# Performance work log

Hardware: AMD Instinct MI355X
Metric: run time of the kernel (lower is better)

## Reference

```python
import jax, jax.numpy as jnp
import numpy as np


def setup_inputs() -> dict:
    key = jax.random.key(0)
    k1, k2 = jax.random.split(key)
    features = jax.random.normal(k1, (2048, 2, 4096), dtype=jnp.float32)
    labels = jax.random.randint(k2, (2048,), 0, 8)  # int labels 0..7
    return {"features": features, "labels": labels}


def reference(features, labels):
    # contrast_mode='one': anchors are view 0 only
    anchor = features[:, 0]                     # [N, d]
    N, d = anchor.shape
    logp = jax.nn.log_softmax(anchor, axis=1)    # [N, d]
    p = jnp.exp(logp)                            # softmax probs

    # Pairwise symmetric KL via one matmul.
    # F.kl_div(log p, q, reduction='batchmean') on 1-D vectors of length d
    # = sum_k q_k (log q_k - log p_k) / d, so
    # sym_kl(i,j) = (C[i,i] + C[j,j] - C[i,j] - C[j,i]) / (2d)
    # where C[i,j] = sum_k p_i[k] * logp_j[k].
    C = p @ logp.T                               # [N, N]
    diag = jnp.diagonal(C)                       # sum p log p per row
    M = (diag[:, None] + diag[None, :] - C - C.T) / (2.0 * d)

    triu = jnp.triu(jnp.ones((N, N), dtype=bool), k=1)  # unordered pairs i<j
    same = labels[:, None] == labels[None, :]
    same_sum = jnp.sum(jnp.where(triu & same, M, 0.0))
    diff_sum = jnp.sum(jnp.where(triu & ~same, M, 0.0))
    return same_sum / diff_sum
```

## Files before the change

### kernel.cpp

```cpp
#include <hip/hip_runtime.h>
#include <cmath>

#define N_ROWS 2048
#define DIM 4096
#define ROW_STRIDE 8192
#define NCLS 8

__device__ __forceinline__ float wred_sum(float v){
  #pragma unroll
  for(int o=32;o>0;o>>=1) v += __shfl_xor(v,o,64);
  return v;
}
__device__ __forceinline__ float wred_max(float v){
  #pragma unroll
  for(int o=32;o>0;o>>=1) v = fmaxf(v,__shfl_xor(v,o,64));
  return v;
}

__global__ __launch_bounds__(256) void k1_rowstats(
    const float* __restrict__ feat, float* __restrict__ lse,
    float* __restrict__ diag, float* __restrict__ zero_region){
  const int t = threadIdx.x;
  const int row = blockIdx.x;
  if(row < 64){
    float4* z = (float4*)zero_region;
    z[row*256 + t] = make_float4(0.f,0.f,0.f,0.f);
  }
  const float4* x4 = (const float4*)(feat + (size_t)row * ROW_STRIDE);
  float4 v[4];
  #pragma unroll
  for(int k=0;k<4;k++) v[k] = x4[t + k*256];

  __shared__ float red[4];
  float m = -INFINITY;
  #pragma unroll
  for(int k=0;k<4;k++)
    m = fmaxf(m, fmaxf(fmaxf(v[k].x,v[k].y), fmaxf(v[k].z,v[k].w)));
  m = wred_max(m);
  if((t & 63)==0) red[t>>6] = m;
  __syncthreads();
  m = fmaxf(fmaxf(red[0],red[1]), fmaxf(red[2],red[3]));
  __syncthreads();
  float s = 0.f;
  #pragma unroll
  for(int k=0;k<4;k++)
    s += __expf(v[k].x - m) + __expf(v[k].y - m)
       + __expf(v[k].z - m) + __expf(v[k].w - m);
  s = wred_sum(s);
  if((t&63)==0) red[t>>6] = s;
  __syncthreads();
  s = red[0]+red[1]+red[2]+red[3];
  __syncthreads();
  const float l = m + __logf(s);
  float dg = 0.f;
  #pragma unroll
  for(int k=0;k<4;k++){
    float a=v[k].x-l, b=v[k].y-l, c=v[k].z-l, d2=v[k].w-l;
    dg += a*__expf(a) + b*__expf(b) + c*__expf(c) + d2*__expf(d2);
  }
  dg = wred_sum(dg);
  if((t&63)==0) red[t>>6] = dg;
  __syncthreads();
  if(t==0){
    lse[row] = l;
    diag[row] = red[0]+red[1]+red[2]+red[3];
  }
}

__global__ __launch_bounds__(256) void k2_accum(
    const float* __restrict__ feat, const float* __restrict__ lse,
    const int* __restrict__ labels,
    float* __restrict__ Pbuf, float* __restrict__ Lbuf){
  const int d = blockIdx.x * 256 + threadIdx.x;
  const int r0 = blockIdx.y * 64;
  float P0=0,P1=0,P2=0,P3=0,P4=0,P5=0,P6=0,P7=0;
  float L0=0,L1=0,L2=0,L3=0,L4=0,L5=0,L6=0,L7=0;
  const float* col = feat + (size_t)r0 * ROW_STRIDE + d;
  #pragma unroll 4
  for(int i=0;i<64;i++){
    const int r = r0 + i;
    float x = col[(size_t)i * ROW_STRIDE];
    float v = x - lse[r];
    float e = __expf(v);
    int lab = __builtin_amdgcn_readfirstlane(labels[r]);
    switch(lab){
      case 0: P0+=e; L0+=v; break;
      case 1: P1+=e; L1+=v; break;
      case 2: P2+=e; L2+=v; break;
      case 3: P3+=e; L3+=v; break;
      case 4: P4+=e; L4+=v; break;
      case 5: P5+=e; L5+=v; break;
      case 6: P6+=e; L6+=v; break;
      default: P7+=e; L7+=v; break;
    }
  }
  atomicAdd(&Pbuf[0*DIM+d],P0); atomicAdd(&Lbuf[0*DIM+d],L0);
  atomicAdd(&Pbuf[1*DIM+d],P1); atomicAdd(&Lbuf[1*DIM+d],L1);
  atomicAdd(&Pbuf[2*DIM+d],P2); atomicAdd(&Lbuf[2*DIM+d],L2);
  atomicAdd(&Pbuf[3*DIM+d],P3); atomicAdd(&Lbuf[3*DIM+d],L3);
  atomicAdd(&Pbuf[4*DIM+d],P4); atomicAdd(&Lbuf[4*DIM+d],L4);
  atomicAdd(&Pbuf[5*DIM+d],P5); atomicAdd(&Lbuf[5*DIM+d],L5);
  atomicAdd(&Pbuf[6*DIM+d],P6); atomicAdd(&Lbuf[6*DIM+d],L6);
  atomicAdd(&Pbuf[7*DIM+d],P7); atomicAdd(&Lbuf[7*DIM+d],L7);
}

__global__ __launch_bounds__(256) void k3_final(
    const float* __restrict__ diag, const int* __restrict__ labels,
    const float* __restrict__ Pbuf, const float* __restrict__ Lbuf,
    float* __restrict__ out){
  const int t = threadIdx.x;
  const int wave = t>>6, lane = t&63;
  double Dl[8]; int Nl[8];
  #pragma unroll
  for(int c=0;c<8;c++){ Dl[c]=0.0; Nl[c]=0; }
  for(int i=t;i<N_ROWS;i+=256){
    int lab = labels[i];
    double dg = (double)diag[i];
    #pragma unroll
    for(int c=0;c<8;c++){
      if(lab==c){ Dl[c]+=dg; Nl[c]++; }
    }
  }
  #pragma unroll
  for(int c=0;c<8;c++){
    #pragma unroll
    for(int o=32;o>0;o>>=1){
      Dl[c] += __shfl_xor(Dl[c],o,64);
      Nl[c] += __shfl_xor(Nl[c],o,64);
    }
  }
  __shared__ double sD[4][8];
  __shared__ int    sN[4][8];
  if(lane==0){
    #pragma unroll
    for(int c=0;c<8;c++){ sD[wave][c]=Dl[c]; sN[wave][c]=Nl[c]; }
  }
  __syncthreads();
  __shared__ double D[8]; __shared__ int Ncnt[8];
  if(t<8){
    D[t]    = sD[0][t]+sD[1][t]+sD[2][t]+sD[3][t];
    Ncnt[t] = sN[0][t]+sN[1][t]+sN[2][t]+sN[3][t];
  }
  __syncthreads();

  double acc_same=0.0, acc_all=0.0;
  for(int dd=t; dd<DIM; dd+=256){
    double ps=0.0, ls=0.0;
    #pragma unroll
    for(int c=0;c<8;c++){
      float p  = Pbuf[c*DIM+dd];
      float lq = Lbuf[c*DIM+dd];
      acc_same += (double)p*(double)lq;
      ps += (double)p; ls += (double)lq;
    }
    acc_all += ps*ls;
  }
  #pragma unroll
  for(int o=32;o>0;o>>=1){
    acc_same += __shfl_xor(acc_same,o,64);
    acc_all  += __shfl_xor(acc_all,o,64);
  }
  __shared__ double sS[4], sA[4];
  if(lane==0){ sS[wave]=acc_same; sA[wave]=acc_all; }
  __syncthreads();
  if(t==0){
    double S_same = sS[0]+sS[1]+sS[2]+sS[3];
    double S_all  = sA[0]+sA[1]+sA[2]+sA[3];
    double same_num=0.0, diff_num=0.0;
    for(int c=0;c<8;c++){
      same_num += (double)Ncnt[c]*D[c];
      diff_num += (double)(N_ROWS - Ncnt[c])*D[c];
    }
    same_num -= S_same;
    diff_num -= (S_all - S_same);
    out[0] = (float)(same_num/diff_num);
  }
}

extern "C" void kernel_launch(void* const* d_in, const int* in_sizes, int n_in,
                              void* d_out, int out_size, void* d_ws, size_t ws_size,
                              hipStream_t stream){
  const float* feat   = (const float*)d_in[0];
  const int*   labels = (const int*)d_in[1];
  float* out = (float*)d_out;
  float* ws  = (float*)d_ws;
  float* lse  = ws;
  float* diag = ws + N_ROWS;
  float* Pbuf = ws + 2*N_ROWS;
  float* Lbuf = Pbuf + NCLS*DIM;

  k1_rowstats<<<N_ROWS, 256, 0, stream>>>(feat, lse, diag, Pbuf);
  k2_accum<<<dim3(DIM/256, 32), 256, 0, stream>>>(feat, lse, labels, Pbuf, Lbuf);
  k3_final<<<1, 256, 0, stream>>>(diag, labels, Pbuf, Lbuf, out);
}
```

Baseline: 131.7 us.

## Fuse final reduction into accumulation kernel via last-block counter

Merges the single-block final kernel into the accumulation kernel: each block increments a global counter after its atomics, and the last block to arrive runs the final reduction. This removes one kernel launch and its gap. It also reuses exp values in the row-stats kernel instead of recomputing them for the diagonal term, and stages per-row lse and labels in shared memory with deeper unrolling. The counter is reset inside the first kernel and ordering relies on threadfences, which adds some synchronization risk.

```diff
diff --git a/kernel.cpp b/kernel.cpp
--- a/kernel.cpp
+++ b/kernel.cpp
@@ -5,6 +5,7 @@
 #define DIM 4096
 #define ROW_STRIDE 8192
 #define NCLS 8
+#define K2_BLOCKS (DIM/256 * 32)
 
 __device__ __forceinline__ float wred_sum(float v){
   #pragma unroll
@@ -19,12 +20,15 @@
 
 __global__ __launch_bounds__(256) void k1_rowstats(
     const float* __restrict__ feat, float* __restrict__ lse,
-    float* __restrict__ diag, float* __restrict__ zero_region){
+    float* __restrict__ diag, float* __restrict__ zero_region,
+    unsigned int* __restrict__ counter){
   const int t = threadIdx.x;
   const int row = blockIdx.x;
   if(row < 64){
     float4* z = (float4*)zero_region;
     z[row*256 + t] = make_float4(0.f,0.f,0.f,0.f);
+  } else if(row == 64 && t == 0){
+    *counter = 0u;
   }
   const float4* x4 = (const float4*)(feat + (size_t)row * ROW_STRIDE);
   float4 v[4];
@@ -41,48 +45,64 @@
   __syncthreads();
   m = fmaxf(fmaxf(red[0],red[1]), fmaxf(red[2],red[3]));
   __syncthreads();
+  float4 e[4];
   float s = 0.f;
   #pragma unroll
-  for(int k=0;k<4;k++)
-    s += __expf(v[k].x - m) + __expf(v[k].y - m)
-       + __expf(v[k].z - m) + __expf(v[k].w - m);
+  for(int k=0;k<4;k++){
+    e[k].x = __expf(v[k].x - m); e[k].y = __expf(v[k].y - m);
+    e[k].z = __expf(v[k].z - m); e[k].w = __expf(v[k].w - m);
+    s += e[k].x + e[k].y + e[k].z + e[k].w;
+  }
   s = wred_sum(s);
   if((t&63)==0) red[t>>6] = s;
   __syncthreads();
   s = red[0]+red[1]+red[2]+red[3];
   __syncthreads();
-  const float l = m + __logf(s);
+  const float ls = __logf(s);
   float dg = 0.f;
   #pragma unroll
   for(int k=0;k<4;k++){
-    float a=v[k].x-l, b=v[k].y-l, c=v[k].z-l, d2=v[k].w-l;
-    dg += a*__expf(a) + b*__expf(b) + c*__expf(c) + d2*__expf(d2);
+    dg += (v[k].x - m - ls)*e[k].x + (v[k].y - m - ls)*e[k].y
+        + (v[k].z - m - ls)*e[k].z + (v[k].w - m - ls)*e[k].w;
   }
   dg = wred_sum(dg);
   if((t&63)==0) red[t>>6] = dg;
   __syncthreads();
   if(t==0){
-    lse[row] = l;
-    diag[row] = red[0]+red[1]+red[2]+red[3];
-  }
-}
-
-__global__ __launch_bounds__(256) void k2_accum(
+    lse[row] = m + ls;
+    diag[row] = (red[0]+red[1]+red[2]+red[3]) / s;
+  }
+}
+
+__global__ __launch_bounds__(256) void k2_accum_final(
     const float* __restrict__ feat, const float* __restrict__ lse,
     const int* __restrict__ labels,
-    float* __restrict__ Pbuf, float* __restrict__ Lbuf){
-  const int d = blockIdx.x * 256 + threadIdx.x;
+    float* __restrict__ Pbuf, float* __restrict__ Lbuf,
+    const float* __restrict__ diag, unsigned int* __restrict__ counter,
+    float* __restrict__ out){
+  const int t = threadIdx.x;
+  const int d = blockIdx.x * 256 + t;
   const int r0 = blockIdx.y * 64;
+
+  __shared__ float s_lse[64];
+  __shared__ int   s_lab[64];
+  if(t < 64){
+    s_lse[t] = lse[r0 + t];
+    s_lab[t] = labels[r0 + t];
+  }
+  __syncthreads();
+
   float P0=0,P1=0,P2=0,P3=0,P4=0,P5=0,P6=0,P7=0;
   float L0=0,L1=0,L2=0,L3=0,L4=0,L5=0,L6=0,L7=0;
-  const float* col = feat + (size_t)r0 * ROW_STRIDE + d;
-  #pragma unroll 4
+
+  const float* base = feat + (size_t)r0 * ROW_STRIDE + d;
+  #pragma unroll 8
   for(int i=0;i<64;i++){
-    const int r = r0 + i;
-    float x = col[(size_t)i * ROW_STRIDE];
-    float v = x - lse[r];
+    float x = base[(size_t)i * ROW_STRIDE];
+    float l = s_lse[i];
+    int lab = __builtin_amdgcn_readfirstlane(s_lab[i]);
+    float v = x - l;
     float e = __expf(v);
-    int lab = __builtin_amdgcn_readfirstlane(labels[r]);
     switch(lab){
       case 0: P0+=e; L0+=v; break;
       case 1: P1+=e; L1+=v; break;
@@ -91,7 +111,7 @@
       case 4: P4+=e; L4+=v; break;
       case 5: P5+=e; L5+=v; break;
       case 6: P6+=e; L6+=v; break;
-      default: P7+=e; L7+=v; break;
+      default:P7+=e; L7+=v; break;
     }
   }
   atomicAdd(&Pbuf[0*DIM+d],P0); atomicAdd(&Lbuf[0*DIM+d],L0);
@@ -102,13 +122,17 @@
   atomicAdd(&Pbuf[5*DIM+d],P5); atomicAdd(&Lbuf[5*DIM+d],L5);
   atomicAdd(&Pbuf[6*DIM+d],P6); atomicAdd(&Lbuf[6*DIM+d],L6);
   atomicAdd(&Pbuf[7*DIM+d],P7); atomicAdd(&Lbuf[7*DIM+d],L7);
-}
-
-__global__ __launch_bounds__(256) void k3_final(
-    const float* __restrict__ diag, const int* __restrict__ labels,
-    const float* __restrict__ Pbuf, const float* __restrict__ Lbuf,
-    float* __restrict__ out){
-  const int t = threadIdx.x;
+
+  __threadfence();
+  __shared__ bool is_last;
+  if(t == 0){
+    unsigned int old = atomicAdd(counter, 1u);
+    is_last = (old == K2_BLOCKS - 1);
+  }
+  __syncthreads();
+  if(!is_last) return;
+  __threadfence();
+
   const int wave = t>>6, lane = t&63;
   double Dl[8]; int Nl[8];
   #pragma unroll
@@ -145,15 +169,15 @@
 
   double acc_same=0.0, acc_all=0.0;
   for(int dd=t; dd<DIM; dd+=256){
-    double ps=0.0, ls=0.0;
+    double ps=0.0, lsum=0.0;
     #pragma unroll
     for(int c=0;c<8;c++){
       float p  = Pbuf[c*DIM+dd];
       float lq = Lbuf[c*DIM+dd];
       acc_same += (double)p*(double)lq;
-      ps += (double)p; ls += (double)lq;
-    }
-    acc_all += ps*ls;
+      ps += (double)p; lsum += (double)lq;
+    }
+    acc_all += ps*lsum;
   }
   #pragma unroll
   for(int o=32;o>0;o>>=1){
@@ -188,8 +212,9 @@
   float* diag = ws + N_ROWS;
   float* Pbuf = ws + 2*N_ROWS;
   float* Lbuf = Pbuf + NCLS*DIM;
-
-  k1_rowstats<<<N_ROWS, 256, 0, stream>>>(feat, lse, diag, Pbuf);
-  k2_accum<<<dim3(DIM/256, 32), 256, 0, stream>>>(feat, lse, labels, Pbuf, Lbuf);
-  k3_final<<<1, 256, 0, stream>>>(diag, labels, Pbuf, Lbuf, out);
-}
+  unsigned int* counter = (unsigned int*)(Lbuf + NCLS*DIM);
+
+  k1_rowstats<<<N_ROWS, 256, 0, stream>>>(feat, lse, diag, Pbuf, counter);
+  k2_accum_final<<<dim3(DIM/256, 32), 256, 0, stream>>>(
+      feat, lse, labels, Pbuf, Lbuf, diag, counter, out);
+}
```

Measured after the change: 165.6 us. 25.8% more time.
